# Kernel tuning notes

Hardware: AMD Instinct MI355X
Metric: run time of the kernel (lower is better)

## Reference

```python
import jax, jax.numpy as jnp
import numpy as np

BS, NA, NC, G = 64, 3, 80, 44
IMG = 352
STRIDE = IMG / G  # 8.0
ANCHORS = np.array([[10.0, 13.0], [16.0, 30.0], [33.0, 23.0]], dtype=np.float32)
SCALED_ANCHORS = ANCHORS / STRIDE  # anchors in grid units


def setup_inputs() -> dict:
    key = jax.random.key(0)
    x = jax.random.normal(key, (BS, NA * (5 + NC), G, G), dtype=jnp.float32)
    return {"x": x}


def reference(x):
    bs = x.shape[0]
    # [bs, nA, 5+nC, H, W] -> [bs, nA, H, W, 5+nC]
    pred = x.reshape(bs, NA, 5 + NC, G, G).transpose(0, 1, 3, 4, 2)
    px = jax.nn.sigmoid(pred[..., 0])
    py = jax.nn.sigmoid(pred[..., 1])
    pw = pred[..., 2]
    ph = pred[..., 3]
    conf = jax.nn.sigmoid(pred[..., 4])
    pred_cls = jax.nn.sigmoid(pred[..., 5:])

    grid = jnp.arange(G, dtype=jnp.float32)
    grid_x = grid[None, None, None, :]          # broadcast over W
    grid_y = grid[None, None, :, None]          # broadcast over H
    aw = jnp.asarray(SCALED_ANCHORS[:, 0])[None, :, None, None]
    ah = jnp.asarray(SCALED_ANCHORS[:, 1])[None, :, None, None]

    bx = px + grid_x
    by = py + grid_y
    bw = jnp.exp(pw) * aw
    bh = jnp.exp(ph) * ah
    pred_boxes = jnp.stack([bx, by, bw, bh], axis=-1)  # [bs,nA,H,W,4]

    out = jnp.concatenate(
        [
            pred_boxes.reshape(bs, -1, 4) * jnp.float32(STRIDE),
            conf.reshape(bs, -1, 1),
            pred_cls.reshape(bs, -1, NC),
        ],
        axis=-1,
    )  # [bs, nA*G*G, 5+nC]
    return out
```

## Files before the change

kernel.cpp:

```cpp
#include <hip/hip_runtime.h>


#define BSZ      64
#define NA       3
#define NC       80
#define GRID     44
#define SPATIAL  (GRID * GRID)
#define CH       (5 + NC)
#define TILE     64
#define TILES_PER_BA ((SPATIAL + TILE - 1) / TILE)
#define LDS_STRIDE   (TILE + 1)
#define STRIDE_F 8.0f

__device__ __forceinline__ float sigf(float x) {
    return 1.0f / (1.0f + __expf(-x));
}

__global__ __launch_bounds__(256, 4)
void yolo_kernel(const float* __restrict__ in, float* __restrict__ out) {
    __shared__ float tile[CH * LDS_STRIDE];

    const int bid = blockIdx.x;
    const int t   = bid % TILES_PER_BA;
    const int ba  = bid / TILES_PER_BA;
    const int a   = ba % NA;

    const int s0    = t * TILE;
    const int valid = min(TILE, SPATIAL - s0);

    const float aw = (a == 0) ? 10.0f : (a == 1) ? 16.0f : 33.0f;
    const float ah = (a == 0) ? 13.0f : (a == 1) ? 30.0f : 23.0f;

    const int tid  = threadIdx.x;
    const int lane = tid & 63;

    const float* inbase = in + (size_t)ba * CH * SPATIAL + s0;
    for (int c = tid >> 6; c < CH; c += 4) {
        if (lane < valid) {
            float v = inbase[(size_t)c * SPATIAL + lane];
            if (c == 0) {
                int gx = (s0 + lane) % GRID;
                v = (sigf(v) + (float)gx) * STRIDE_F;
            } else if (c == 1) {
                int gy = (s0 + lane) / GRID;
                v = (sigf(v) + (float)gy) * STRIDE_F;
            } else if (c == 2) {
                v = __expf(v) * aw;
            } else if (c == 3) {
                v = __expf(v) * ah;
            } else {
                v = sigf(v);
            }
            tile[c * LDS_STRIDE + lane] = v;
        }
    }
    __syncthreads();

    const size_t obase = ((size_t)ba * SPATIAL + s0) * CH;
    const int total = valid * CH;
    for (int k = tid; k < total; k += 256) {
        int s = k / CH;
        int c = k - s * CH;
        out[obase + k] = tile[c * LDS_STRIDE + s];
    }
}

extern "C" void kernel_launch(void* const* d_in, const int* in_sizes, int n_in,
                              void* d_out, int out_size, void* d_ws, size_t ws_size,
                              hipStream_t stream) {
    const float* in = (const float*)d_in[0];
    float* out = (float*)d_out;
    const int grid = BSZ * NA * TILES_PER_BA;
    yolo_kernel<<<grid, 256, 0, stream>>>(in, out);
}
```

Measured before the change: 244.7 us.

## Restructure YOLO decode into per-wave 16-point tiles with float4 I/O and prefetch

Each wave now handles 4 consecutive 16-point spatial tiles. Input loads are float4 and double-buffered in registers, so the next tile's loads are issued while the current one is processed. Each wave transposes through its own LDS slice, which removes the block-wide barrier, and writes its contiguous output chunk with coalesced float4 stores. The cost is more registers and an unrolled, branchy per-element channel selection. The launch bound also rises to 6 blocks per CU.

```diff
diff --git a/kernel.cpp b/kernel.cpp
--- a/kernel.cpp
+++ b/kernel.cpp
@@ -1,67 +1,91 @@
 #include <hip/hip_runtime.h>
 
 
-#define BSZ      64
 #define NA       3
 #define NC       80
-#define GRID     44
-#define SPATIAL  (GRID * GRID)
+#define GRIDW    44
+#define SPATIAL  (GRIDW * GRIDW)
 #define CH       (5 + NC)
-#define TILE     64
-#define TILES_PER_BA ((SPATIAL + TILE - 1) / TILE)
-#define LDS_STRIDE   (TILE + 1)
+#define TS       16
+#define TPB      (SPATIAL / TS)
+#define NT       4
+#define NW       4
+#define TOTT     (64 * NA * TPB)
+#define NBLK     (TOTT / (NT * NW))
 #define STRIDE_F 8.0f
 
 __device__ __forceinline__ float sigf(float x) {
     return 1.0f / (1.0f + __expf(-x));
 }
 
-__global__ __launch_bounds__(256, 4)
+__global__ __launch_bounds__(256, 6)
 void yolo_kernel(const float* __restrict__ in, float* __restrict__ out) {
-    __shared__ float tile[CH * LDS_STRIDE];
-
-    const int bid = blockIdx.x;
-    const int t   = bid % TILES_PER_BA;
-    const int ba  = bid / TILES_PER_BA;
-    const int a   = ba % NA;
-
-    const int s0    = t * TILE;
-    const int valid = min(TILE, SPATIAL - s0);
-
-    const float aw = (a == 0) ? 10.0f : (a == 1) ? 16.0f : 33.0f;
-    const float ah = (a == 0) ? 13.0f : (a == 1) ? 30.0f : 23.0f;
+    __shared__ float lds[NW][TS * CH];
 
     const int tid  = threadIdx.x;
+    const int w    = tid >> 6;
     const int lane = tid & 63;
+    const int cg   = lane >> 2;
+    const int sq   = (lane & 3) * 4;
 
-    const float* inbase = in + (size_t)ba * CH * SPATIAL + s0;
-    for (int c = tid >> 6; c < CH; c += 4) {
-        if (lane < valid) {
-            float v = inbase[(size_t)c * SPATIAL + lane];
-            if (c == 0) {
-                int gx = (s0 + lane) % GRID;
-                v = (sigf(v) + (float)gx) * STRIDE_F;
-            } else if (c == 1) {
-                int gy = (s0 + lane) / GRID;
-                v = (sigf(v) + (float)gy) * STRIDE_F;
-            } else if (c == 2) {
-                v = __expf(v) * aw;
-            } else if (c == 3) {
-                v = __expf(v) * ah;
-            } else {
-                v = sigf(v);
+    const int t0 = (blockIdx.x * NW + w) * NT;
+    float* const myld = lds[w];
+
+    float4 buf[2][6];
+
+    auto load_tile = [&](int T, float4* d) {
+        int ba = T / TPB;
+        int tl = T - ba * TPB;
+        const float* ib = in + (size_t)ba * CH * SPATIAL + tl * TS;
+        #pragma unroll
+        for (int j = 0; j < 6; ++j) {
+            int c = j * 16 + cg;
+            if (j < 5 || cg < 5)
+                d[j] = *(const float4*)(ib + (size_t)c * SPATIAL + sq);
+        }
+    };
+
+    load_tile(t0, buf[0]);
+
+    #pragma unroll
+    for (int it = 0; it < NT; ++it) {
+        const int T = t0 + it;
+        if (it + 1 < NT) load_tile(T + 1, buf[(it + 1) & 1]);
+
+        float4* cur = buf[it & 1];
+        const int ba = T / TPB;
+        const int tl = T - ba * TPB;
+        const int s0 = tl * TS;
+        const int a  = ba % NA;
+        const float aw = (a == 0) ? 10.0f : (a == 1) ? 16.0f : 33.0f;
+        const float ah = (a == 0) ? 13.0f : (a == 1) ? 30.0f : 23.0f;
+
+        #pragma unroll
+        for (int j = 0; j < 6; ++j) {
+            if (j == 5 && cg >= 5) continue;
+            int c = j * 16 + cg;
+            float r[4] = {cur[j].x, cur[j].y, cur[j].z, cur[j].w};
+            #pragma unroll
+            for (int e = 0; e < 4; ++e) {
+                int   s = sq + e;
+                float x = r[e];
+                float o;
+                if (c == 0)      { int gs = s0 + s; o = (sigf(x) + (float)(gs % GRIDW)) * STRIDE_F; }
+                else if (c == 1) { int gs = s0 + s; o = (sigf(x) + (float)(gs / GRIDW)) * STRIDE_F; }
+                else if (c == 2) o = __expf(x) * aw;
+                else if (c == 3) o = __expf(x) * ah;
+                else             o = sigf(x);
+                myld[s * CH + c] = o;
             }
-            tile[c * LDS_STRIDE + lane] = v;
         }
-    }
-    __syncthreads();
 
-    const size_t obase = ((size_t)ba * SPATIAL + s0) * CH;
-    const int total = valid * CH;
-    for (int k = tid; k < total; k += 256) {
-        int s = k / CH;
-        int c = k - s * CH;
-        out[obase + k] = tile[c * LDS_STRIDE + s];
+        float* ob = out + (size_t)T * (TS * CH);
+        #pragma unroll
+        for (int i = 0; i < 6; ++i) {
+            int k4 = lane + i * 64;
+            if (k4 < 340)
+                *(float4*)(ob + k4 * 4) = *(const float4*)(myld + k4 * 4);
+        }
     }
 }
 
@@ -70,6 +94,5 @@
                               hipStream_t stream) {
     const float* in = (const float*)d_in[0];
     float* out = (float*)d_out;
-    const int grid = BSZ * NA * TILES_PER_BA;
-    yolo_kernel<<<grid, 256, 0, stream>>>(in, out);
+    yolo_kernel<<<NBLK, 256, 0, stream>>>(in, out);
 }
```

New measurement: 237.6 us. -2.9%, faster.
